# Optimization experiments

Hardware: AMD Instinct MI355X
Metric: run time of the kernel (lower is better)

## Reference

```python
import jax, jax.numpy as jnp
import numpy as np

B, C, QK, T, S = 16, 256, 32, 15, 31


def _conv1x1(x, w, b):
    # 1x1 conv as channel matmul; w: [out, in]
    return jnp.einsum("oc,bchw->bohw", w, x) + b[None, :, None, None]


def _spatial_attn(x, qw, qb, kw, kb, vw, vb, g):
    Bn, Cn, H, W = x.shape
    N = H * W
    q = _conv1x1(x, qw, qb).reshape(Bn, -1, N)  # [B,QK,N]
    k = _conv1x1(x, kw, kb).reshape(Bn, -1, N)  # [B,QK,N]
    v = _conv1x1(x, vw, vb).reshape(Bn, Cn, N)  # [B,C,N]
    energy = jnp.einsum("bqn,bqm->bnm", q, k)   # [B,N,N]
    A = jax.nn.softmax(energy, axis=-1)
    out = g * jnp.einsum("bcm,bnm->bcn", v, A)
    return out.reshape(Bn, Cn, H, W)


def _channel_attn_calc(x):
    Bn, Cn = x.shape[0], x.shape[1]
    f = x.reshape(Bn, Cn, -1)
    e = jnp.einsum("bcn,bdn->bcd", f, f)  # [B,C,C]
    e = jnp.max(e, axis=-1, keepdims=True) - e
    return jax.nn.softmax(e, axis=-1)


def _channel_attn_use(x, A, w):
    Bn, Cn = x.shape[0], x.shape[1]
    v = x.reshape(Bn, Cn, -1)
    return (w * jnp.einsum("bcd,bdn->bcn", A, v)).reshape(x.shape)


def _mod_deform_conv(x, ow, ob, w, b):
    # Modulated deformable conv (DCNv2) 3x3, pad 1, stride 1.
    Bn, Cn, H, W = x.shape
    om = jax.lax.conv_general_dilated(x, ow, (1, 1), ((1, 1), (1, 1)),
                                      dimension_numbers=("NCHW", "OIHW", "NCHW"))
    om = om + ob[None, :, None, None]  # [B,27,H,W]
    off_y, off_x, mask = om[:, :9], om[:, 9:18], jax.nn.sigmoid(om[:, 18:])
    ky, kx = jnp.meshgrid(jnp.arange(3), jnp.arange(3), indexing="ij")
    py = off_y + jnp.arange(H)[None, None, :, None] + (ky.reshape(9) - 1)[None, :, None, None]
    px = off_x + jnp.arange(W)[None, None, None, :] + (kx.reshape(9) - 1)[None, :, None, None]
    y0f = jnp.floor(py); x0f = jnp.floor(px)
    wy = py - y0f; wx = px - x0f
    y0 = y0f.astype(jnp.int32); x0 = x0f.astype(jnp.int32)
    xf = x.reshape(Bn, Cn, H * W)

    def gather(yi, xi, wgt):
        valid = (yi >= 0) & (yi < H) & (xi >= 0) & (xi < W)
        idx = (jnp.clip(yi, 0, H - 1) * W + jnp.clip(xi, 0, W - 1)).reshape(Bn, -1)
        g = jax.vmap(lambda a, i: a[:, i])(xf, idx).reshape(Bn, Cn, 9, H, W)
        return g * (wgt * valid.astype(x.dtype))[:, None]

    val = (gather(y0, x0, (1 - wy) * (1 - wx)) + gather(y0, x0 + 1, (1 - wy) * wx)
           + gather(y0 + 1, x0, wy * (1 - wx)) + gather(y0 + 1, x0 + 1, wy * wx))
    val = val * mask[:, None]  # [B,C,9,H,W]
    return jnp.einsum("bckhw,ock->bohw", val, w.reshape(w.shape[0], Cn, 9)) + b[None, :, None, None]


def _forward(template_features, sr_features,
             t_sp_qw, t_sp_qb, t_sp_kw, t_sp_kb, t_sp_vw, t_sp_vb, t_sp_g,
             s_sp_qw, s_sp_qb, s_sp_kw, s_sp_kb, s_sp_vw, s_sp_vb, s_sp_g,
             w_t_ch, w_s_ch, w_s2t, w_t2s,
             t_off_w, t_off_b, t_dcn_w, t_dcn_b,
             s_off_w, s_off_b, s_dcn_w, s_dcn_b):
    t, s = template_features, sr_features
    t_sp = _spatial_attn(t, t_sp_qw, t_sp_qb, t_sp_kw, t_sp_kb, t_sp_vw, t_sp_vb, t_sp_g)
    s_sp = _spatial_attn(s, s_sp_qw, s_sp_qb, s_sp_kw, s_sp_kb, s_sp_vw, s_sp_vb, s_sp_g)
    tA = _channel_attn_calc(t)
    sA = _channel_attn_calc(s)
    t_ch = _channel_attn_use(t, tA, w_t_ch)
    s_ch = _channel_attn_use(s, sA, w_s_ch)
    t_x = _channel_attn_use(t, sA, w_s2t)   # sr->template cross attention
    s_x = _channel_attn_use(s, tA, w_t2s)   # template->sr cross attention
    t_out = t + t_sp + t_ch + t_x
    s_out = s + s_sp + s_ch + s_x
    t_out = _mod_deform_conv(t_out, t_off_w, t_off_b, t_dcn_w, t_dcn_b)
    s_out = _mod_deform_conv(s_out, s_off_w, s_off_b, s_dcn_w, s_dcn_b)
    return t_out, s_out


def setup_inputs() -> dict:
    key = jax.random.key(0)
    ks = jax.random.split(key, 28)
    r = lambda i, shape, sc=0.05: jax.random.normal(ks[i], shape, dtype=jnp.float32) * sc
    return {
        "template_features": jax.random.normal(ks[0], (B, C, T, T), dtype=jnp.float32),
        "sr_features": jax.random.normal(ks[1], (B, C, S, S), dtype=jnp.float32),
        "t_sp_qw": r(2, (QK, C)), "t_sp_qb": r(3, (QK,)),
        "t_sp_kw": r(4, (QK, C)), "t_sp_kb": r(5, (QK,)),
        "t_sp_vw": r(6, (C, C)), "t_sp_vb": r(7, (C,)), "t_sp_g": r(8, (1,), 0.5),
        "s_sp_qw": r(9, (QK, C)), "s_sp_qb": r(10, (QK,)),
        "s_sp_kw": r(11, (QK, C)), "s_sp_kb": r(12, (QK,)),
        "s_sp_vw": r(13, (C, C)), "s_sp_vb": r(14, (C,)), "s_sp_g": r(15, (1,), 0.5),
        "w_t_ch": r(16, (1,), 0.5), "w_s_ch": r(17, (1,), 0.5),
        "w_s2t": r(18, (1,), 0.5), "w_t2s": r(19, (1,), 0.5),
        "t_off_w": r(20, (27, C, 3, 3), 0.01), "t_off_b": r(21, (27,), 0.01),
        "t_dcn_w": r(22, (C, C, 3, 3)), "t_dcn_b": r(23, (C,)),
        "s_off_w": r(24, (27, C, 3, 3), 0.01), "s_off_b": r(25, (27,), 0.01),
        "s_dcn_w": r(26, (C, C, 3, 3)), "s_dcn_b": r(27, (C,)),
    }


def reference(template_features, sr_features,
              t_sp_qw, t_sp_qb, t_sp_kw, t_sp_kb, t_sp_vw, t_sp_vb, t_sp_g,
              s_sp_qw, s_sp_qb, s_sp_kw, s_sp_kb, s_sp_vw, s_sp_vb, s_sp_g,
              w_t_ch, w_s_ch, w_s2t, w_t2s,
              t_off_w, t_off_b, t_dcn_w, t_dcn_b,
              s_off_w, s_off_b, s_dcn_w, s_dcn_b):
    return _forward(template_features, sr_features,
                    t_sp_qw, t_sp_qb, t_sp_kw, t_sp_kb, t_sp_vw, t_sp_vb, t_sp_g,
                    s_sp_qw, s_sp_qb, s_sp_kw, s_sp_kb, s_sp_vw, s_sp_vb, s_sp_g,
                    w_t_ch, w_s_ch, w_s2t, w_t2s,
                    t_off_w, t_off_b, t_dcn_w, t_dcn_b,
                    s_off_w, s_off_b, s_dcn_w, s_dcn_b)
```

## Files before the change

### kernel.cpp

```cpp
#include <hip/hip_runtime.h>
#include <hip/hip_bf16.h>
#include <cmath>

typedef __attribute__((ext_vector_type(8))) short bf16x8;
typedef __attribute__((ext_vector_type(4))) float f32x4;

__device__ inline ushort f2bf(float f) {
  __hip_bfloat16 h = __float2bfloat16(f);
  return *reinterpret_cast<ushort*>(&h);
}
__device__ inline float bf2f(ushort u) {
  return __uint_as_float((uint)u << 16);
}
__device__ inline float bflo(uint x) { return __uint_as_float(x << 16); }
__device__ inline float bfhi(uint x) { return __uint_as_float(x & 0xffff0000u); }

__device__ inline bool fdecode(int totalS, int gxS, int gyS, int gxT, int gyT,
                               int& bx, int& by, int& bz, bool& isT) {
  const int total = gridDim.x;
  const int id = blockIdx.x;
  int wid = (id & 7) * (total >> 3) + (id >> 3);
  const int totalT = gxT * gyT * 16;
  if (wid >= totalS + totalT) return false;
  isT = wid >= totalS;
  int lid = isT ? wid - totalS : wid;
  const int gx = isT ? gxT : gxS;
  const int gy = isT ? gyT : gyS;
  bx = lid % gx;
  lid /= gx;
  by = lid % gy;
  bz = lid / gy;
  return true;
}

__device__ inline void vdecode(int v, int vtotal, int totalS, int gxS, int gyS,
                               int gxT, int gyT, int& bx, int& by, int& bz,
                               bool& isT) {
  int wid = (v & 7) * (vtotal >> 3) + (v >> 3);
  isT = wid >= totalS;
  int lid = isT ? wid - totalS : wid;
  const int gx = isT ? gxT : gxS;
  const int gy = isT ? gyT : gyS;
  bx = lid % gx;
  lid /= gx;
  by = lid % gy;
  bz = lid / gy;
}

__global__ __launch_bounds__(256) void prep_cast_fused_kernel(
    const float* __restrict__ t_qw, const float* __restrict__ t_qb,
    const float* __restrict__ t_kw, const float* __restrict__ t_kb,
    const float* __restrict__ s_qw, const float* __restrict__ s_qb,
    const float* __restrict__ s_kw, const float* __restrict__ s_kb,
    const float* __restrict__ t_vw, const float* __restrict__ t_vb,
    const float* __restrict__ s_vw, const float* __restrict__ s_vb,
    const float* __restrict__ t_off_w, const float* __restrict__ s_off_w,
    const float* __restrict__ t_dcn_w, const float* __restrict__ s_dcn_w,
    ushort* __restrict__ Wall_t, ushort* __restrict__ Wall_s,
    float* __restrict__ biasAll_t, float* __restrict__ biasAll_s,
    ushort* __restrict__ owb_t, ushort* __restrict__ owb_s,
    ushort* __restrict__ Awb_t, ushort* __restrict__ Awb_s,
    const float* __restrict__ xS, ushort* __restrict__ oS,
    ushort* __restrict__ pS, int NS_, int NRS_, int NpS_,
    const float* __restrict__ xT, ushort* __restrict__ oT,
    ushort* __restrict__ pT, int NT_, int NRT_, int NpT_) {
  __shared__ float T[64][65];
  const int tid = threadIdx.x;
  const int vid = blockIdx.x;
  if (vid < 5832) {
    int i = vid * 256 + tid;
    if (i < 81920) {
      const int r = i >> 8, c = i & 255;
      float v;
      if (r < 256) v = t_vw[(size_t)r * 256 + c];
      else if (r < 288) v = t_qw[(size_t)(r - 256) * 256 + c];
      else v = t_kw[(size_t)(r - 288) * 256 + c];
      Wall_t[i] = f2bf(v);
      return;
    }
    i -= 81920;
    if (i < 81920) {
      const int r = i >> 8, c = i & 255;
      float v;
      if (r < 256) v = s_vw[(size_t)r * 256 + c];
      else if (r < 288) v = s_qw[(size_t)(r - 256) * 256 + c];
      else v = s_kw[(size_t)(r - 288) * 256 + c];
      Wall_s[i] = f2bf(v);
      return;
    }
    i -= 81920;
    if (i < 320) {
      biasAll_t[i] = (i < 256) ? t_vb[i] : ((i < 288) ? t_qb[i - 256] : t_kb[i - 288]);
      return;
    }
    i -= 320;
    if (i < 320) {
      biasAll_s[i] = (i < 256) ? s_vb[i] : ((i < 288) ? s_qb[i - 256] : s_kb[i - 288]);
      return;
    }
    i -= 320;
    if (i < 73728) {
      const int o = i / 2304, k = i % 2304, tap = k >> 8, c = k & 255;
      owb_t[i] = (o < 27) ? f2bf(t_off_w[(size_t)o * 2304 + c * 9 + tap]) : (ushort)0;
      return;
    }
    i -= 73728;
    if (i < 73728) {
      const int o = i / 2304, k = i % 2304, tap = k >> 8, c = k & 255;
      owb_s[i] = (o < 27) ? f2bf(s_off_w[(size_t)o * 2304 + c * 9 + tap]) : (ushort)0;
      return;
    }
    i -= 73728;
    if (i < 589824) {
      const int frag = i >> 9, within = i & 511;
      const int lane = within >> 3, j = within & 7;
      const int mt = frag / 72, kt = frag % 72;
      const int o = mt * 16 + (lane & 15);
      const int k = kt * 32 + (lane >> 4) * 8 + j;
      const int tap = k >> 8, c = k & 255;
      Awb_t[i] = f2bf(t_dcn_w[(size_t)o * 2304 + c * 9 + tap]);
      return;
    }
    i -= 589824;
    if (i < 589824) {
      const int frag = i >> 9, within = i & 511;
      const int lane = within >> 3, j = within & 7;
      const int mt = frag / 72, kt = frag % 72;
      const int o = mt * 16 + (lane & 15);
      const int k = kt * 32 + (lane >> 4) * 8 + j;
      const int tap = k >> 8, c = k & 255;
      Awb_s[i] = f2bf(s_dcn_w[(size_t)o * 2304 + c * 9 + tap]);
    }
    return;
  }
  constexpr int C = 256;
  int bx, by, bz; bool isT;
  vdecode(vid - 5832, 1280, 1024, 16, 4, 4, 4, bx, by, bz, isT);
  const float* x = isT ? xT : xS;
  ushort* xTo = isT ? oT : oS;
  ushort* xbf = isT ? pT : pS;
  const int N = isT ? NT_ : NS_;
  const int NR = isT ? NRT_ : NRS_;
  const int Np = isT ? NpT_ : NpS_;
  const int b = bz;
  const int n0 = bx * 64, c0 = by * 64;
  const float* xb = x + (size_t)b * C * N;
  for (int u = tid; u < 4096; u += 256) {
    const int cc = u >> 6, nn = u & 63;
    const int gn = n0 + nn;
    T[cc][nn] = (gn < N) ? xb[(size_t)(c0 + cc) * N + gn] : 0.f;
  }
  __syncthreads();
  ushort* ob = xTo + (size_t)b * NR * C;
  for (int u = tid; u < 4096; u += 256) {
    const int nn = u >> 6, cc = u & 63;
    ob[(size_t)(n0 + nn) * C + c0 + cc] = f2bf(T[cc][nn]);
  }
  ushort* pb = xbf + (size_t)b * C * Np;
  for (int u = tid; u < 4096; u += 256) {
    const int cc = u >> 6, nn = u & 63;
    const int gn = n0 + nn;
    if (gn < Np) pb[(size_t)(c0 + cc) * Np + gn] = f2bf(T[cc][nn]);
  }
}

__global__ __launch_bounds__(256) void proj_gram_fused_kernel(
    const ushort* __restrict__ WallS, const float* __restrict__ bS,
    const ushort* __restrict__ BtS, ushort* __restrict__ vS,
    float* __restrict__ qkS, int NS_, int NpS_, int NRS_,
    const ushort* __restrict__ WallT, const float* __restrict__ bT,
    const ushort* __restrict__ BtT, ushort* __restrict__ vT,
    float* __restrict__ qkT, int NT_, int NpT_, int NRT_,
    const ushort* __restrict__ xbfS, float* __restrict__ AscP, int KpS_,
    const ushort* __restrict__ xbfT, float* __restrict__ AtcP, int KpT_) {
  constexpr int C = 256;
  __shared__ ushort Asm[128][40];
  __shared__ ushort Bsm[64][40];
  const int tid = threadIdx.x, lane = tid & 63, w = tid >> 6;
  const int vid = blockIdx.x;
  if (vid < 1600) {
    int bx, by, bz; bool isT;
    vdecode(vid, 1600, 1280, 16, 5, 4, 5, bx, by, bz, isT);
    const ushort* Wall = isT ? WallT : WallS;
    const float* bias = isT ? bT : bS;
    const ushort* Bt = isT ? BtT : BtS;
    ushort* vbf = isT ? vT : vS;
    float* qk = isT ? qkT : qkS;
    const int N = isT ? NT_ : NS_, Np = isT ? NpT_ : NpS_, NR = isT ? NRT_ : NRS_;
    const int n0 = bx * 64, m0 = by * 64, b = bz;
    const ushort* Ab = Wall + (size_t)m0 * C;
    const ushort* Bb = Bt + (size_t)b * NR * C;
    f32x4 acc[4];
#pragma unroll
    for (int i = 0; i < 4; i++) acc[i] = (f32x4){0.f, 0.f, 0.f, 0.f};
    for (int k0 = 0; k0 < C; k0 += 32) {
      {
        const int row = tid >> 2, seg = tid & 3;
        *reinterpret_cast<uint4*>(&Asm[row][seg * 8]) =
            *reinterpret_cast<const uint4*>(&Ab[(size_t)row * C + k0 + seg * 8]);
        *reinterpret_cast<uint4*>(&Bsm[row][seg * 8]) =
            *reinterpret_cast<const uint4*>(&Bb[(size_t)(n0 + row) * C + k0 + seg * 8]);
      }
      __syncthreads();
      const int koff = (lane >> 4) * 8;
      const bf16x8 bfr = *reinterpret_cast<const bf16x8*>(&Bsm[w * 16 + (lane & 15)][koff]);
#pragma unroll
      for (int mf = 0; mf < 4; mf++) {
        const bf16x8 af = *reinterpret_cast<const bf16x8*>(&Asm[mf * 16 + (lane & 15)][koff]);
        acc[mf] = __builtin_amdgcn_mfma_f32_16x16x32_bf16(af, bfr, acc[mf], 0, 0, 0);
      }
      __syncthreads();
    }
    const int gn = n0 + w * 16 + (lane & 15);
#pragma unroll
    for (int mf = 0; mf < 4; mf++) {
      const int mbase = m0 + mf * 16 + ((lane >> 4) * 4);
#pragma unroll
      for (int rr = 0; rr < 4; rr++) {
        const int m = mbase + rr;
        if (m < 256) {
          if (gn < Np) {
            ushort v = (gn < N) ? f2bf(acc[mf][rr] + bias[m]) : (ushort)0;
            vbf[((size_t)b * 256 + m) * Np + gn] = v;
          }
        } else {
          if (gn < N)
            qk[((size_t)b * 64 + (m - 256)) * N + gn] = acc[mf][rr] + bias[m];
        }
      }
    }
    return;
  }
  {
    constexpr int BM = 128, NW = 4, NF = 2, WN = 2;
    int bx, by, bz; bool isT;
    vdecode(vid - 1600, 256, 128, 4, 2, 4, 2, bx, by, bz, isT);
    const ushort* A = isT ? xbfT : xbfS;
    float* outF = isT ? AtcP : AscP;
    const int Kp = isT ? KpT_ : KpS_;
    const int n0 = bx * 64, m0 = by * BM, b = bz;
    const ushort* Ab = A + (size_t)b * C * Kp;
    const int wr = w / WN, wc = w % WN;
    f32x4 acc[4][NF];
#pragma unroll
    for (int i = 0; i < 4; i++)
#pragma unroll
      for (int j = 0; j < NF; j++) acc[i][j] = (f32x4){0.f, 0.f, 0.f, 0.f};
    for (int k0 = 0; k0 < Kp; k0 += 32) {
      for (int u = tid; u < BM * 4; u += NW * 64) {
        const int row = u >> 2, seg = u & 3;
        *reinterpret_cast<uint4*>(&Asm[row][seg * 8]) =
            *reinterpret_cast<const uint4*>(&Ab[(size_t)(m0 + row) * Kp + k0 + seg * 8]);
      }
      for (int u = tid; u < 64 * 4; u += NW * 64) {
        const int row = u >> 2, seg = u & 3;
        *reinterpret_cast<uint4*>(&Bsm[row][seg * 8]) =
            *reinterpret_cast<const uint4*>(&Ab[(size_t)(n0 + row) * Kp + k0 + seg * 8]);
      }
      __syncthreads();
      const int koff = (lane >> 4) * 8;
      bf16x8 af[4], bfr[NF];
#pragma unroll
      for (int mf = 0; mf < 4; mf++)
        af[mf] = *reinterpret_cast<const bf16x8*>(&Asm[wr * 64 + mf * 16 + (lane & 15)][koff]);
#pragma unroll
      for (int nf = 0; nf < NF; nf++)
        bfr[nf] = *reinterpret_cast<const bf16x8*>(&Bsm[wc * NF * 16 + nf * 16 + (lane & 15)][koff]);
#pragma unroll
      for (int mf = 0; mf < 4; mf++)
#pragma unroll
        for (int nf = 0; nf < NF; nf++)
          acc[mf][nf] = __builtin_amdgcn_mfma_f32_16x16x32_bf16(af[mf], bfr[nf], acc[mf][nf], 0, 0, 0);
      __syncthreads();
    }
#pragma unroll
    for (int mf = 0; mf < 4; mf++) {
      const int mbase = m0 + wr * 64 + mf * 16 + ((lane >> 4) * 4);
#pragma unroll
      for (int nf = 0; nf < NF; nf++) {
        const int gn = n0 + wc * NF * 16 + nf * 16 + (lane & 15);
#pragma unroll
        for (int rr = 0; rr < 4; rr++)
          outF[((size_t)b * C + mbase + rr) * C + gn] = acc[mf][nf][rr];
      }
    }
  }
}

__global__ __launch_bounds__(256) void energy_mcomb_fused_kernel(
    const float* __restrict__ qkS, ushort* __restrict__ SS, int NS_, int NpS_,
    const float* __restrict__ qkT, ushort* __restrict__ ST, int NT_, int NpT_,
    const float* __restrict__ Atc, const float* __restrict__ Asc,
    const float* __restrict__ w_t_ch, const float* __restrict__ w_s2t,
    const float* __restrict__ w_s_ch, const float* __restrict__ w_t2s,
    ushort* __restrict__ Mc_t, ushort* __restrict__ Mc_s) {
  __shared__ ushort Aq[64][40];
  __shared__ ushort Bk[64][40];
  __shared__ float red[8];
  const int tid = threadIdx.x;
  const int vid = blockIdx.x;
  if (vid < 4352) {
    int bx, by, bz; bool isT;
    vdecode(vid, 4352, 4096, 16, 16, 4, 4, bx, by, bz, isT);
    const float* qk = isT ? qkT : qkS;
    ushort* Sbf = isT ? ST : SS;
    const int N = isT ? NT_ : NS_, Np = isT ? NpT_ : NpS_;
    const int m0 = bx * 64, n0 = by * 64, b = bz;
    const float* qb = qk + (size_t)b * 64 * N;
    const float* kb = qb + (size_t)32 * N;
    const int lane = tid & 63, w = tid >> 6;
    for (int u = tid; u < 2048; u += 256) {
      const int c = u >> 6, nn = u & 63;
      const int gn = n0 + nn, gm = m0 + nn;
      Aq[nn][c] = (gn < N) ? f2bf(qb[(size_t)c * N + gn]) : (ushort)0;
      Bk[nn][c] = (gm < N) ? f2bf(kb[(size_t)c * N + gm]) : (ushort)0;
    }
    __syncthreads();
    const int koff = (lane >> 4) * 8;
    const bf16x8 af = *reinterpret_cast<const bf16x8*>(&Aq[w * 16 + (lane & 15)][koff]);
    f32x4 acc[4];
#pragma unroll
    for (int j = 0; j < 4; j++) {
      const bf16x8 bf = *reinterpret_cast<const bf16x8*>(&Bk[j * 16 + (lane & 15)][koff]);
      acc[j] = __builtin_amdgcn_mfma_f32_16x16x32_bf16(af, bf, (f32x4){0.f, 0.f, 0.f, 0.f}, 0, 0, 0);
    }
#pragma unroll
    for (int j = 0; j < 4; j++) {
      const int m = m0 + j * 16 + (lane & 15);
      if (m >= Np) continue;
#pragma unroll
      for (int r = 0; r < 4; r++) {
        const int n = n0 + w * 16 + (lane >> 4) * 4 + r;
        if (n < N) Sbf[((size_t)b * N + n) * Np + m] = (m < N) ? f2bf(acc[j][r]) : (ushort)0;
      }
    }
    return;
  }
  {
    const int row = vid - 4352;
    const size_t idx = (size_t)row * 256 + tid;
    const float a = -Atc[idx];
    const float s = -Asc[idx];
    float ma = a, ms = s;
#pragma unroll
    for (int off = 32; off; off >>= 1) {
      ma = fmaxf(ma, __shfl_xor(ma, off, 64));
      ms = fmaxf(ms, __shfl_xor(ms, off, 64));
    }
    if ((tid & 63) == 0) { red[tid >> 6] = ma; red[4 + (tid >> 6)] = ms; }
    __syncthreads();
    if (tid == 0) {
      float m1 = red[0], m2 = red[4];
      for (int i = 1; i < 4; i++) { m1 = fmaxf(m1, red[i]); m2 = fmaxf(m2, red[4 + i]); }
      red[0] = m1; red[4] = m2;
    }
    __syncthreads();
    ma = red[0]; ms = red[4];
    __syncthreads();
    const float ea = __expf(a - ma), es = __expf(s - ms);
    float sa = ea, ss = es;
#pragma unroll
    for (int off = 32; off; off >>= 1) {
      sa += __shfl_xor(sa, off, 64);
      ss += __shfl_xor(ss, off, 64);
    }
    if ((tid & 63) == 0) { red[tid >> 6] = sa; red[4 + (tid >> 6)] = ss; }
    __syncthreads();
    if (tid == 0) {
      float t1 = 0.f, t2 = 0.f;
      for (int i = 0; i < 4; i++) { t1 += red[i]; t2 += red[4 + i]; }
      red[0] = t1; red[4] = t2;
    }
    __syncthreads();
    const float Pa = ea / red[0], Ps = es / red[4];
    Mc_t[idx] = f2bf(w_t_ch[0] * Pa + w_s2t[0] * Ps);
    Mc_s[idx] = f2bf(w_s_ch[0] * Ps + w_t2s[0] * Pa);
  }
}

__global__ __launch_bounds__(256) void softmax_bf16_fused_kernel(
    ushort* __restrict__ Ss, int Ns, int Nps, ushort* __restrict__ St, int Nt,
    int Npt, int rowsS) {
  __shared__ float buf[992];
  __shared__ float red[4];
  const int row = blockIdx.x;
  ushort* r;
  int N;
  if (row < rowsS) {
    r = Ss + (size_t)row * Nps;
    N = Ns;
  } else {
    r = St + (size_t)(row - rowsS) * Npt;
    N = Nt;
  }
  const int tid = threadIdx.x;
  float mx = -1e30f;
  for (int i = tid; i < N; i += 256) {
    float f = bf2f(r[i]);
    buf[i] = f;
    mx = fmaxf(mx, f);
  }
#pragma unroll
  for (int off = 32; off; off >>= 1) mx = fmaxf(mx, __shfl_xor(mx, off, 64));
  if ((tid & 63) == 0) red[tid >> 6] = mx;
  __syncthreads();
  if (tid == 0) {
    float m2 = red[0];
    for (int i = 1; i < 4; i++) m2 = fmaxf(m2, red[i]);
    red[0] = m2;
  }
  __syncthreads();
  mx = red[0];
  __syncthreads();
  float s = 0.f;
  for (int i = tid; i < N; i += 256) {
    float v = __expf(buf[i] - mx);
    buf[i] = v;
    s += v;
  }
#pragma unroll
  for (int off = 32; off; off >>= 1) s += __shfl_xor(s, off, 64);
  if ((tid & 63) == 0) red[tid >> 6] = s;
  __syncthreads();
  if (tid == 0) {
    float t = 0.f;
    for (int i = 0; i < 4; i++) t += red[i];
    red[0] = t;
  }
  __syncthreads();
  const float inv = 1.f / red[0];
  for (int i = tid; i < N; i += 256) r[i] = f2bf(buf[i] * inv);
}

__global__ __launch_bounds__(256) void pv_chan_fused_kernel(
    const ushort* __restrict__ vS, const ushort* __restrict__ SS,
    const ushort* __restrict__ McS, const ushort* __restrict__ xTS,
    const float* __restrict__ xS, const float* __restrict__ gS,
    ushort* __restrict__ xsTS, int NS_, int NpS_, int NRS_,
    const ushort* __restrict__ vT, const ushort* __restrict__ ST,
    const ushort* __restrict__ McT, const ushort* __restrict__ xTT,
    const float* __restrict__ xT_, const float* __restrict__ gT,
    ushort* __restrict__ xsTT, int NT_, int NpT_, int NRT_) {
  constexpr int C = 256, BM = 128, NW = 4, NF = 2, WN = 2;
  __shared__ ushort Asm[BM][40];
  __shared__ ushort Bsm[64][40];
  int bx, by, bz; bool isT;
  if (!fdecode(512, 16, 2, 4, 2, bx, by, bz, isT)) return;
  const ushort* vbf = isT ? vT : vS;
  const ushort* Sbf = isT ? ST : SS;
  const ushort* Mc = isT ? McT : McS;
  const ushort* xTb = isT ? xTT : xTS;
  const float* x = isT ? xT_ : xS;
  const float* gp = isT ? gT : gS;
  ushort* xsT = isT ? xsTT : xsTS;
  const int N = isT ? NT_ : NS_, Np = isT ? NpT_ : NpS_;
  const int NR = isT ? NRT_ : NRS_;
  const int n0 = bx * 64, m0 = by * BM, b = bz;
  const int tid = threadIdx.x, lane = tid & 63, w = tid >> 6;
  const int wr = w / WN, wc = w % WN;
  f32x4 acc[4][NF];
#pragma unroll
  for (int i = 0; i < 4; i++)
#pragma unroll
    for (int j = 0; j < NF; j++) acc[i][j] = (f32x4){0.f, 0.f, 0.f, 0.f};
  const int koff = (lane >> 4) * 8;
  {
    const ushort* Ab = vbf + (size_t)b * C * Np;
    const ushort* Bb = Sbf + (size_t)b * (size_t)N * Np;
    for (int k0 = 0; k0 < Np; k0 += 32) {
      for (int u = tid; u < BM * 4; u += NW * 64) {
        const int row = u >> 2, seg = u & 3;
        *reinterpret_cast<uint4*>(&Asm[row][seg * 8]) =
            *reinterpret_cast<const uint4*>(&Ab[(size_t)(m0 + row) * Np + k0 + seg * 8]);
      }
      for (int u = tid; u < 64 * 4; u += NW * 64) {
        const int row = u >> 2, seg = u & 3;
        const int gn = n0 + row;
        uint4 val;
        if (gn < N)
          val = *reinterpret_cast<const uint4*>(&Bb[(size_t)gn * Np + k0 + seg * 8]);
        else
          val = make_uint4(0, 0, 0, 0);
        *reinterpret_cast<uint4*>(&Bsm[row][seg * 8]) = val;
      }
      __syncthreads();
      bf16x8 af[4], bfr[NF];
#pragma unroll
      for (int mf = 0; mf < 4; mf++)
        af[mf] = *reinterpret_cast<const bf16x8*>(&Asm[wr * 64 + mf * 16 + (lane & 15)][koff]);
#pragma unroll
      for (int nf = 0; nf < NF; nf++)
        bfr[nf] = *reinterpret_cast<const bf16x8*>(&Bsm[wc * NF * 16 + nf * 16 + (lane & 15)][koff]);
#pragma unroll
      for (int mf = 0; mf < 4; mf++)
#pragma unroll
        for (int nf = 0; nf < NF; nf++)
          acc[mf][nf] = __builtin_amdgcn_mfma_f32_16x16x32_bf16(af[mf], bfr[nf], acc[mf][nf], 0, 0, 0);
      __syncthreads();
    }
  }
  const float g = *gp;
#pragma unroll
  for (int mf = 0; mf < 4; mf++)
#pragma unroll
    for (int nf = 0; nf < NF; nf++)
#pragma unroll
      for (int rr = 0; rr < 4; rr++) acc[mf][nf][rr] *= g;
  {
    const ushort* Ab = Mc + (size_t)b * C * C;
    const ushort* Bb = xTb + (size_t)b * NR * C;
    for (int k0 = 0; k0 < C; k0 += 32) {
      for (int u = tid; u < BM * 4; u += NW * 64) {
        const int row = u >> 2, seg = u & 3;
        *reinterpret_cast<uint4*>(&Asm[row][seg * 8]) =
            *reinterpret_cast<const uint4*>(&Ab[(size_t)(m0 + row) * C + k0 + seg * 8]);
      }
      for (int u = tid; u < 64 * 4; u += NW * 64) {
        const int row = u >> 2, seg = u & 3;
        *reinterpret_cast<uint4*>(&Bsm[row][seg * 8]) =
            *reinterpret_cast<const uint4*>(&Bb[(size_t)(n0 + row) * C + k0 + seg * 8]);
      }
      __syncthreads();
      bf16x8 af[4], bfr[NF];
#pragma unroll
      for (int mf = 0; mf < 4; mf++)
        af[mf] = *reinterpret_cast<const bf16x8*>(&Asm[wr * 64 + mf * 16 + (lane & 15)][koff]);
#pragma unroll
      for (int nf = 0; nf < NF; nf++)
        bfr[nf] = *reinterpret_cast<const bf16x8*>(&Bsm[wc * NF * 16 + nf * 16 + (lane & 15)][koff]);
#pragma unroll
      for (int mf = 0; mf < 4; mf++)
#pragma unroll
        for (int nf = 0; nf < NF; nf++)
          acc[mf][nf] = __builtin_amdgcn_mfma_f32_16x16x32_bf16(af[mf], bfr[nf], acc[mf][nf], 0, 0, 0);
      __syncthreads();
    }
  }
#pragma unroll
  for (int mf = 0; mf < 4; mf++) {
    const int mbase = m0 + wr * 64 + mf * 16 + ((lane >> 4) * 4);
#pragma unroll
    for (int nf = 0; nf < NF; nf++) {
      const int gn = n0 + wc * NF * 16 + nf * 16 + (lane & 15);
      if (gn < N) {
        float s[4];
#pragma unroll
        for (int rr = 0; rr < 4; rr++)
          s[rr] = x[((size_t)b * C + mbase + rr) * N + gn] + acc[mf][nf][rr];
        uint lo = (uint)f2bf(s[0]) | ((uint)f2bf(s[1]) << 16);
        uint hi = (uint)f2bf(s[2]) | ((uint)f2bf(s[3]) << 16);
        *reinterpret_cast<uint2*>(&xsT[((size_t)b * NR + gn) * C + mbase]) =
            make_uint2(lo, hi);
      }
    }
  }
}

__global__ __launch_bounds__(256) void offconv_prep_fused_kernel(
    const ushort* __restrict__ xS, const ushort* __restrict__ owS,
    const float* __restrict__ obS, uint4* __restrict__ prS, int HS_, int WS_,
    int NS_, int NRS_,
    const ushort* __restrict__ xT, const ushort* __restrict__ owT,
    const float* __restrict__ obT, uint4* __restrict__ prT, int HT_, int WT_,
    int NT_, int NRT_) {
  __shared__ ushort Asm[32][136];
  __shared__ ushort Bsm[64][136];
  __shared__ int qsrc[64];
  __shared__ float som[27][65];
  int bx, by, bz; bool isT;
  if (!fdecode(256, 16, 1, 4, 1, bx, by, bz, isT)) return;
  const ushort* xsT = isT ? xT : xS;
  const ushort* owb = isT ? owT : owS;
  const float* ob = isT ? obT : obS;
  uint4* prep = isT ? prT : prS;
  const int H = isT ? HT_ : HS_, Wd = isT ? WT_ : WS_;
  const int N = isT ? NT_ : NS_, NR = isT ? NRT_ : NRS_;
  const int n0 = bx * 64, b = bz;
  const int tid = threadIdx.x, lane = tid & 63, w = tid >> 6;
  const ushort* xb = xsT + (size_t)b * NR * 256;
  f32x4 acc[2];
  acc[0] = (f32x4){0.f, 0.f, 0.f, 0.f};
  acc[1] = (f32x4){0.f, 0.f, 0.f, 0.f};
  for (int tap = 0; tap < 9; ++tap) {
    const int dy = tap / 3 - 1, dx = tap - (tap / 3) * 3 - 1;
    if (tid < 64) {
      const int p = n0 + tid;
      int q = -1;
      if (p < N) {
        const int h = p / Wd, ww = p - (p / Wd) * Wd;
        const int yy = h + dy, xx = ww + dx;
        if (yy >= 0 && yy < H && xx >= 0 && xx < Wd) q = yy * Wd + xx;
      }
      qsrc[tid] = q;
    }
    __syncthreads();
#pragma unroll
    for (int half = 0; half < 2; ++half) {
      const int k0 = tap * 256 + half * 128;
      for (int u = tid; u < 512; u += 256) {
        const int row = u >> 4, seg = u & 15;
        *reinterpret_cast<uint4*>(&Asm[row][seg * 8]) =
            *reinterpret_cast<const uint4*>(&owb[(size_t)row * 2304 + k0 + seg * 8]);
      }
      for (int u = tid; u < 1024; u += 256) {
        const int row = u >> 4, seg = u & 15;
        const int q = qsrc[row];
        uint4 val = make_uint4(0, 0, 0, 0);
        if (q >= 0)
          val = *reinterpret_cast<const uint4*>(&xb[(size_t)q * 256 + half * 128 + seg * 8]);
        *reinterpret_cast<uint4*>(&Bsm[row][seg * 8]) = val;
      }
      __syncthreads();
#pragma unroll
      for (int sub = 0; sub < 4; ++sub) {
        const int koff = sub * 32 + (lane >> 4) * 8;
        const bf16x8 b0 = *reinterpret_cast<const bf16x8*>(&Bsm[w * 16 + (lane & 15)][koff]);
#pragma unroll
        for (int mf = 0; mf < 2; ++mf) {
          const bf16x8 a0 = *reinterpret_cast<const bf16x8*>(&Asm[mf * 16 + (lane & 15)][koff]);
          acc[mf] = __builtin_amdgcn_mfma_f32_16x16x32_bf16(a0, b0, acc[mf], 0, 0, 0);
        }
      }
      __syncthreads();
    }
  }
#pragma unroll
  for (int mf = 0; mf < 2; ++mf) {
#pragma unroll
    for (int r = 0; r < 4; ++r) {
      const int o = mf * 16 + (lane >> 4) * 4 + r;
      const int n = w * 16 + (lane & 15);
      if (o < 27) som[o][n] = acc[mf][r] + ob[o];
    }
  }
  __syncthreads();
  for (int u = tid; u < 576; u += 256) {
    const int tap = u / 64, pp = u - (u / 64) * 64;
    const int p = n0 + pp;
    if (p >= N) continue;
    const float offy = som[tap][pp];
    const float offx = som[9 + tap][pp];
    const float mraw = som[18 + tap][pp];
    const float mval = 1.f / (1.f + __expf(-mraw));
    const int ky = tap / 3, kx = tap - (tap / 3) * 3;
    const int h = p / Wd, ww = p - (p / Wd) * Wd;
    const float py = offy + (float)(h + ky - 1);
    const float px = offx + (float)(ww + kx - 1);
    const float y0f = floorf(py), x0f = floorf(px);
    const float wy = py - y0f, wx = px - x0f;
    const int y0 = (int)y0f, x0 = (int)x0f;
    const int ys0 = min(max(y0, 0), H - 2);
    const int xs0 = min(max(x0, 0), Wd - 2);
    const float wr0 = (ys0 == y0) ? (1.f - wy) : ((ys0 == y0 + 1) ? wy : 0.f);
    const float wr1 = (ys0 + 1 == y0) ? (1.f - wy) : ((ys0 + 1 == y0 + 1) ? wy : 0.f);
    const float wc0 = (xs0 == x0) ? (1.f - wx) : ((xs0 == x0 + 1) ? wx : 0.f);
    const float wc1 = (xs0 + 1 == x0) ? (1.f - wx) : ((xs0 + 1 == x0 + 1) ? wx : 0.f);
    const float w00 = wr0 * wc0 * mval, w01 = wr0 * wc1 * mval;
    const float w10 = wr1 * wc0 * mval, w11 = wr1 * wc1 * mval;
    uint4 pk;
    pk.x = (uint)(ys0 * Wd + xs0);
    pk.y = (uint)f2bf(w00) | ((uint)f2bf(w01) << 16);
    pk.z = (uint)f2bf(w10) | ((uint)f2bf(w11) << 16);
    pk.w = 0;
    prep[((size_t)b * 9 + tap) * N + p] = pk;
  }
}

__global__ __launch_bounds__(512) void dcn_fused_kernel(
    const ushort* __restrict__ xS, const uint4* __restrict__ prS,
    const ushort* __restrict__ AwS, const float* __restrict__ biS,
    float* __restrict__ oS, int NS_, int WS_, int NRS_,
    const ushort* __restrict__ xT, const uint4* __restrict__ prT,
    const ushort* __restrict__ AwT, const float* __restrict__ biT,
    float* __restrict__ oT, int NT_, int WT_, int NRT_) {
  constexpr int C = 256, MF = 4;
  __shared__ ushort Bsm[32][72];
  __shared__ int sq[32];
  __shared__ float swl[4][32];
  int bx, by, bz; bool isT;
  if (!fdecode(512, 32, 1, 8, 1, bx, by, bz, isT)) return;
  const ushort* xsT = isT ? xT : xS;
  const uint4* prep = isT ? prT : prS;
  const ushort* Awb = isT ? AwT : AwS;
  const float* bias = isT ? biT : biS;
  float* out = isT ? oT : oS;
  const int N = isT ? NT_ : NS_, Wd = isT ? WT_ : WS_, NR = isT ? NRT_ : NRS_;
  const int n0 = bx * 32, b = bz;
  const int tid = threadIdx.x, lane = tid & 63, w = tid >> 6;
  const int wr = w >> 1, wc = w & 1;
  const ushort* xb = xsT + (size_t)b * NR * C;
  const int un0 = tid >> 5;
  const int un1 = un0 + 16;
  const int kk2 = (tid & 31) * 2;
  f32x4 acc[MF];
#pragma unroll
  for (int i = 0; i < MF; i++) acc[i] = (f32x4){0.f, 0.f, 0.f, 0.f};
  uint bReg[2][4];
  int sqr0 = 0, sqr1 = 0;
  float w0a[4], w1a[4];
  const size_t rowYp = (size_t)Wd * C;
  for (int tap = 0; tap < 9; ++tap) {
    if (tid < 32) {
      const int p = n0 + tid;
      if (p < N) {
        const uint4 pk = prep[((size_t)b * 9 + tap) * N + p];
        sq[tid] = (int)pk.x * C;
        swl[0][tid] = bf2f((ushort)(pk.y & 0xffff));
        swl[1][tid] = bf2f((ushort)(pk.y >> 16));
        swl[2][tid] = bf2f((ushort)(pk.z & 0xffff));
        swl[3][tid] = bf2f((ushort)(pk.z >> 16));
      } else {
        sq[tid] = 0;
        swl[0][tid] = swl[1][tid] = swl[2][tid] = swl[3][tid] = 0.f;
      }
    }
    __syncthreads();
    sqr0 = sq[un0];
    sqr1 = sq[un1];
#pragma unroll
    for (int q = 0; q < 4; q++) {
      w0a[q] = swl[q][un0];
      w1a[q] = swl[q][un1];
    }
    {
      const ushort* pA = xb + sqr0 + kk2;
      bReg[0][0] = *reinterpret_cast<const uint*>(pA);
      bReg[0][1] = *reinterpret_cast<const uint*>(pA + C);
      bReg[0][2] = *reinterpret_cast<const uint*>(pA + rowYp);
      bReg[0][3] = *reinterpret_cast<const uint*>(pA + rowYp + C);
      const ushort* pB = xb + sqr1 + kk2;
      bReg[1][0] = *reinterpret_cast<const uint*>(pB);
      bReg[1][1] = *reinterpret_cast<const uint*>(pB + C);
      bReg[1][2] = *reinterpret_cast<const uint*>(pB + rowYp);
      bReg[1][3] = *reinterpret_cast<const uint*>(pB + rowYp + C);
    }
#pragma unroll
    for (int ks = 0; ks < 4; ++ks) {
      bf16x8 afr[2][4];
      const int ktb = tap * 8 + ks * 2;
#pragma unroll
      for (int sub = 0; sub < 2; ++sub)
#pragma unroll
        for (int mf = 0; mf < 4; ++mf)
          afr[sub][mf] = *reinterpret_cast<const bf16x8*>(
              Awb + ((((size_t)(wr * 4 + mf) * 72) + ktb + sub) << 9) + lane * 8);
      {
        const float vlo0 = w0a[0] * bflo(bReg[0][0]) + w0a[1] * bflo(bReg[0][1]) +
                           w0a[2] * bflo(bReg[0][2]) + w0a[3] * bflo(bReg[0][3]);
        const float vhi0 = w0a[0] * bfhi(bReg[0][0]) + w0a[1] * bfhi(bReg[0][1]) +
                           w0a[2] * bfhi(bReg[0][2]) + w0a[3] * bfhi(bReg[0][3]);
        *reinterpret_cast<uint*>(&Bsm[un0][kk2]) =
            (uint)f2bf(vlo0) | ((uint)f2bf(vhi0) << 16);
        const float vlo1 = w1a[0] * bflo(bReg[1][0]) + w1a[1] * bflo(bReg[1][1]) +
                           w1a[2] * bflo(bReg[1][2]) + w1a[3] * bflo(bReg[1][3]);
        const float vhi1 = w1a[0] * bfhi(bReg[1][0]) + w1a[1] * bfhi(bReg[1][1]) +
                           w1a[2] * bfhi(bReg[1][2]) + w1a[3] * bfhi(bReg[1][3]);
        *reinterpret_cast<uint*>(&Bsm[un1][kk2]) =
            (uint)f2bf(vlo1) | ((uint)f2bf(vhi1) << 16);
      }
      __syncthreads();
      if (ks < 3) {
        const int c1 = (ks + 1) * 64;
        const ushort* pA = xb + sqr0 + c1 + kk2;
        bReg[0][0] = *reinterpret_cast<const uint*>(pA);
        bReg[0][1] = *reinterpret_cast<const uint*>(pA + C);
        bReg[0][2] = *reinterpret_cast<const uint*>(pA + rowYp);
        bReg[0][3] = *reinterpret_cast<const uint*>(pA + rowYp + C);
        const ushort* pB = xb + sqr1 + c1 + kk2;
        bReg[1][0] = *reinterpret_cast<const uint*>(pB);
        bReg[1][1] = *reinterpret_cast<const uint*>(pB + C);
        bReg[1][2] = *reinterpret_cast<const uint*>(pB + rowYp);
        bReg[1][3] = *reinterpret_cast<const uint*>(pB + rowYp + C);
      }
#pragma unroll
      for (int sub = 0; sub < 2; ++sub) {
        const int koff = sub * 32 + (lane >> 4) * 8;
        const bf16x8 bfv = *reinterpret_cast<const bf16x8*>(&Bsm[wc * 16 + (lane & 15)][koff]);
#pragma unroll
        for (int mf = 0; mf < MF; mf++)
          acc[mf] = __builtin_amdgcn_mfma_f32_16x16x32_bf16(afr[sub][mf], bfv, acc[mf], 0, 0, 0);
      }
      __syncthreads();
    }
  }
  const int gn = n0 + wc * 16 + (lane & 15);
#pragma unroll
  for (int mf = 0; mf < MF; mf++) {
    const int mbase = wr * 64 + mf * 16 + ((lane >> 4) * 4);
    if (gn < N) {
#pragma unroll
      for (int rr = 0; rr < 4; rr++)
        out[((size_t)b * C + mbase + rr) * N + gn] = acc[mf][rr] + bias[mbase + rr];
    }
  }
}

extern "C" void kernel_launch(void* const* d_in, const int* in_sizes, int n_in,
                              void* d_out, int out_size, void* d_ws, size_t ws_size,
                              hipStream_t stream) {
  const float* t_in = (const float*)d_in[0];
  const float* s_in = (const float*)d_in[1];
  const float* t_qw = (const float*)d_in[2];
  const float* t_qb = (const float*)d_in[3];
  const float* t_kw = (const float*)d_in[4];
  const float* t_kb = (const float*)d_in[5];
  const float* t_vw = (const float*)d_in[6];
  const float* t_vb = (const float*)d_in[7];
  const float* t_g = (const float*)d_in[8];
  const float* s_qw = (const float*)d_in[9];
  const float* s_qb = (const float*)d_in[10];
  const float* s_kw = (const float*)d_in[11];
  const float* s_kb = (const float*)d_in[12];
  const float* s_vw = (const float*)d_in[13];
  const float* s_vb = (const float*)d_in[14];
  const float* s_g = (const float*)d_in[15];
  const float* w_t_ch = (const float*)d_in[16];
  const float* w_s_ch = (const float*)d_in[17];
  const float* w_s2t = (const float*)d_in[18];
  const float* w_t2s = (const float*)d_in[19];
  const float* t_off_w = (const float*)d_in[20];
  const float* t_off_b = (const float*)d_in[21];
  const float* t_dcn_w = (const float*)d_in[22];
  const float* t_dcn_b = (const float*)d_in[23];
  const float* s_off_w = (const float*)d_in[24];
  const float* s_off_b = (const float*)d_in[25];
  const float* s_dcn_w = (const float*)d_in[26];
  const float* s_dcn_b = (const float*)d_in[27];
  (void)in_sizes; (void)n_in; (void)out_size; (void)ws_size;

  constexpr int Bn = 16, C = 256;
  constexpr int HT = 15, WT = 15, NT = HT * WT;
  constexpr int HS = 31, WS2 = 31, NS = HS * WS2;
  constexpr int NpT = 256, NpS = 992;
  constexpr int NRT = 256, NRS = 1024;

  float* ws = (float*)d_ws;
  size_t off = 0;
  auto alloc = [&](size_t n) {
    n = (n + 3) & ~(size_t)3;
    float* p = ws + off; off += n; return p;
  };
  auto allocU = [&](size_t nu) { return (ushort*)alloc((nu + 1) / 2); };

  float* qk_t = alloc((size_t)Bn * 64 * NT);
  float* qk_s = alloc((size_t)Bn * 64 * NS);
  ushort* Wall_t = allocU((size_t)320 * C);
  ushort* Wall_s = allocU((size_t)320 * C);
  float* biasAll_t = alloc(320);
  float* biasAll_s = alloc(320);
  ushort* xT_t = allocU((size_t)Bn * NRT * C);
  ushort* xT_s = allocU((size_t)Bn * NRS * C);
  ushort* xbf_t = allocU((size_t)Bn * C * NpT);
  ushort* xbf_s = allocU((size_t)Bn * C * NpS);
  ushort* v_tbf = allocU((size_t)Bn * C * NpT);
  ushort* v_sbf = allocU((size_t)Bn * C * NpS);
  ushort* S_t = allocU((size_t)Bn * NT * NpT);
  ushort* S_s = allocU((size_t)Bn * NS * NpS);
  ushort* xsT_t = allocU((size_t)Bn * NRT * C);
  ushort* xsT_s = allocU((size_t)Bn * NRS * C);
  float* Atc = alloc((size_t)Bn * C * C);
  float* Asc = alloc((size_t)Bn * C * C);
  ushort* Mc_t = allocU((size_t)Bn * C * C);
  ushort* Mc_s = allocU((size_t)Bn * C * C);
  ushort* owb_t = allocU((size_t)32 * 2304);
  ushort* owb_s = allocU((size_t)32 * 2304);
  ushort* Awb_t = allocU((size_t)256 * 2304);
  ushort* Awb_s = allocU((size_t)256 * 2304);
  uint4* prep_t = (uint4*)alloc((size_t)Bn * 9 * NT * 4);
  uint4* prep_s = (uint4*)alloc((size_t)Bn * 9 * NS * 4);

  dim3 blk(256);

  prep_cast_fused_kernel<<<dim3(5832 + 1280), blk, 0, stream>>>(
      t_qw, t_qb, t_kw, t_kb, s_qw, s_qb, s_kw, s_kb,
      t_vw, t_vb, s_vw, s_vb, t_off_w, s_off_w, t_dcn_w, s_dcn_w,
      Wall_t, Wall_s, biasAll_t, biasAll_s, owb_t, owb_s, Awb_t, Awb_s,
      s_in, xT_s, xbf_s, NS, NRS, NpS, t_in, xT_t, xbf_t, NT, NRT, NpT);

  proj_gram_fused_kernel<<<dim3(1600 + 256), blk, 0, stream>>>(
      Wall_s, biasAll_s, xT_s, v_sbf, qk_s, NS, NpS, NRS,
      Wall_t, biasAll_t, xT_t, v_tbf, qk_t, NT, NpT, NRT,
      xbf_s, Asc, NpS, xbf_t, Atc, NpT);

  energy_mcomb_fused_kernel<<<dim3(4352 + 4096), blk, 0, stream>>>(
      qk_s, S_s, NS, NpS, qk_t, S_t, NT, NpT,
      Atc, Asc, w_t_ch, w_s2t, w_s_ch, w_t2s, Mc_t, Mc_s);

  softmax_bf16_fused_kernel<<<dim3(Bn * NS + Bn * NT), blk, 0, stream>>>(
      S_s, NS, NpS, S_t, NT, NpT, Bn * NS);

  pv_chan_fused_kernel<<<dim3(640), blk, 0, stream>>>(
      v_sbf, S_s, Mc_s, xT_s, s_in, s_g, xsT_s, NS, NpS, NRS,
      v_tbf, S_t, Mc_t, xT_t, t_in, t_g, xsT_t, NT, NpT, NRT);

  offconv_prep_fused_kernel<<<dim3(320), blk, 0, stream>>>(
      xsT_s, owb_s, s_off_b, prep_s, HS, WS2, NS, NRS,
      xsT_t, owb_t, t_off_b, prep_t, HT, WT, NT, NRT);

  float* out_t = (float*)d_out;
  float* out_s = out_t + (size_t)Bn * C * NT;
  dcn_fused_kernel<<<dim3(640), dim3(512), 0, stream>>>(
      xsT_s, prep_s, Awb_s, s_dcn_b, out_s, NS, WS2, NRS,
      xsT_t, prep_t, Awb_t, t_dcn_b, out_t, NT, WT, NRT);
}
```

Before: 273.3 us.

## Fuse spatial softmax into energy and PV kernels via deferred normalization

```diff
diff --git a/kernel.cpp b/kernel.cpp
--- a/kernel.cpp
+++ b/kernel.cpp
@@ -63,7 +63,8 @@
     const float* __restrict__ xS, ushort* __restrict__ oS,
     ushort* __restrict__ pS, int NS_, int NRS_, int NpS_,
     const float* __restrict__ xT, ushort* __restrict__ oT,
-    ushort* __restrict__ pT, int NT_, int NRT_, int NpT_) {
+    ushort* __restrict__ pT, int NT_, int NRT_, int NpT_,
+    float* __restrict__ rsS, float* __restrict__ rsT) {
   __shared__ float T[64][65];
   const int tid = threadIdx.x;
   const int vid = blockIdx.x;
@@ -131,6 +132,12 @@
       const int tap = k >> 8, c = k & 255;
       Awb_s[i] = f2bf(s_dcn_w[(size_t)o * 2304 + c * 9 + tap]);
     }
+    return;
+  }
+  if (vid >= 7112) {
+    int i = (vid - 7112) * 256 + tid;
+    if (i < 15376) rsS[i] = 0.f;
+    else if (i < 18976) rsT[i - 15376] = 0.f;
     return;
   }
   constexpr int C = 256;
@@ -290,6 +297,7 @@
 __global__ __launch_bounds__(256) void energy_mcomb_fused_kernel(
     const float* __restrict__ qkS, ushort* __restrict__ SS, int NS_, int NpS_,
     const float* __restrict__ qkT, ushort* __restrict__ ST, int NT_, int NpT_,
+    float* __restrict__ rsS, float* __restrict__ rsT,
     const float* __restrict__ Atc, const float* __restrict__ Asc,
     const float* __restrict__ w_t_ch, const float* __restrict__ w_s2t,
     const float* __restrict__ w_s_ch, const float* __restrict__ w_t2s,
@@ -304,6 +312,7 @@
     vdecode(vid, 4352, 4096, 16, 16, 4, 4, bx, by, bz, isT);
     const float* qk = isT ? qkT : qkS;
     ushort* Sbf = isT ? ST : SS;
+    float* rowsum = isT ? rsT : rsS;
     const int N = isT ? NT_ : NS_, Np = isT ? NpT_ : NpS_;
     const int m0 = bx * 64, n0 = by * 64, b = bz;
     const float* qb = qk + (size_t)b * 64 * N;
@@ -324,14 +333,29 @@
       const bf16x8 bf = *reinterpret_cast<const bf16x8*>(&Bk[j * 16 + (lane & 15)][koff]);
       acc[j] = __builtin_amdgcn_mfma_f32_16x16x32_bf16(af, bf, (f32x4){0.f, 0.f, 0.f, 0.f}, 0, 0, 0);
     }
+    float psum[4] = {0.f, 0.f, 0.f, 0.f};
 #pragma unroll
     for (int j = 0; j < 4; j++) {
       const int m = m0 + j * 16 + (lane & 15);
-      if (m >= Np) continue;
 #pragma unroll
       for (int r = 0; r < 4; r++) {
         const int n = n0 + w * 16 + (lane >> 4) * 4 + r;
-        if (n < N) Sbf[((size_t)b * N + n) * Np + m] = (m < N) ? f2bf(acc[j][r]) : (ushort)0;
+        float e = 0.f;
+        if (m < N) e = __expf(acc[j][r]);
+        if (m < Np && n < N) Sbf[((size_t)b * N + n) * Np + m] = f2bf(e);
+        psum[r] += e;
+      }
+    }
+#pragma unroll
+    for (int d = 1; d < 16; d <<= 1) {
+#pragma unroll
+      for (int r = 0; r < 4; r++) psum[r] += __shfl_xor(psum[r], d, 64);
+    }
+    if ((lane & 15) == 0) {
+#pragma unroll
+      for (int r = 0; r < 4; r++) {
+        const int n = n0 + w * 16 + (lane >> 4) * 4 + r;
+        if (n < N) atomicAdd(&rowsum[(size_t)b * N + n], psum[r]);
       }
     }
     return;
@@ -378,69 +402,17 @@
   }
 }
 
-__global__ __launch_bounds__(256) void softmax_bf16_fused_kernel(
-    ushort* __restrict__ Ss, int Ns, int Nps, ushort* __restrict__ St, int Nt,
-    int Npt, int rowsS) {
-  __shared__ float buf[992];
-  __shared__ float red[4];
-  const int row = blockIdx.x;
-  ushort* r;
-  int N;
-  if (row < rowsS) {
-    r = Ss + (size_t)row * Nps;
-    N = Ns;
-  } else {
-    r = St + (size_t)(row - rowsS) * Npt;
-    N = Nt;
-  }
-  const int tid = threadIdx.x;
-  float mx = -1e30f;
-  for (int i = tid; i < N; i += 256) {
-    float f = bf2f(r[i]);
-    buf[i] = f;
-    mx = fmaxf(mx, f);
-  }
-#pragma unroll
-  for (int off = 32; off; off >>= 1) mx = fmaxf(mx, __shfl_xor(mx, off, 64));
-  if ((tid & 63) == 0) red[tid >> 6] = mx;
-  __syncthreads();
-  if (tid == 0) {
-    float m2 = red[0];
-    for (int i = 1; i < 4; i++) m2 = fmaxf(m2, red[i]);
-    red[0] = m2;
-  }
-  __syncthreads();
-  mx = red[0];
-  __syncthreads();
-  float s = 0.f;
-  for (int i = tid; i < N; i += 256) {
-    float v = __expf(buf[i] - mx);
-    buf[i] = v;
-    s += v;
-  }
-#pragma unroll
-  for (int off = 32; off; off >>= 1) s += __shfl_xor(s, off, 64);
-  if ((tid & 63) == 0) red[tid >> 6] = s;
-  __syncthreads();
-  if (tid == 0) {
-    float t = 0.f;
-    for (int i = 0; i < 4; i++) t += red[i];
-    red[0] = t;
-  }
-  __syncthreads();
-  const float inv = 1.f / red[0];
-  for (int i = tid; i < N; i += 256) r[i] = f2bf(buf[i] * inv);
-}
-
 __global__ __launch_bounds__(256) void pv_chan_fused_kernel(
     const ushort* __restrict__ vS, const ushort* __restrict__ SS,
-    const ushort* __restrict__ McS, const ushort* __restrict__ xTS,
-    const float* __restrict__ xS, const float* __restrict__ gS,
-    ushort* __restrict__ xsTS, int NS_, int NpS_, int NRS_,
+    const float* __restrict__ rsS, const ushort* __restrict__ McS,
+    const ushort* __restrict__ xTS, const float* __restrict__ xS,
+    const float* __restrict__ gS, ushort* __restrict__ xsTS, int NS_,
+    int NpS_, int NRS_,
     const ushort* __restrict__ vT, const ushort* __restrict__ ST,
-    const ushort* __restrict__ McT, const ushort* __restrict__ xTT,
-    const float* __restrict__ xT_, const float* __restrict__ gT,
-    ushort* __restrict__ xsTT, int NT_, int NpT_, int NRT_) {
+    const float* __restrict__ rsT, const ushort* __restrict__ McT,
+    const ushort* __restrict__ xTT, const float* __restrict__ xT_,
+    const float* __restrict__ gT, ushort* __restrict__ xsTT, int NT_,
+    int NpT_, int NRT_) {
   constexpr int C = 256, BM = 128, NW = 4, NF = 2, WN = 2;
   __shared__ ushort Asm[BM][40];
   __shared__ ushort Bsm[64][40];
@@ -448,6 +420,7 @@
   if (!fdecode(512, 16, 2, 4, 2, bx, by, bz, isT)) return;
   const ushort* vbf = isT ? vT : vS;
   const ushort* Sbf = isT ? ST : SS;
+  const float* rowsum = isT ? rsT : rsS;
   const ushort* Mc = isT ? McT : McS;
   const ushort* xTb = isT ? xTT : xTS;
   const float* x = isT ? xT_ : xS;
@@ -500,12 +473,19 @@
     }
   }
   const float g = *gp;
+  float fac[NF];
+#pragma unroll
+  for (int nf = 0; nf < NF; nf++) {
+    const int gn = n0 + wc * NF * 16 + nf * 16 + (lane & 15);
+    const float rs = (gn < N) ? rowsum[(size_t)b * N + gn] : 1.f;
+    fac[nf] = g / rs;
+  }
 #pragma unroll
   for (int mf = 0; mf < 4; mf++)
 #pragma unroll
     for (int nf = 0; nf < NF; nf++)
 #pragma unroll
-      for (int rr = 0; rr < 4; rr++) acc[mf][nf][rr] *= g;
+      for (int rr = 0; rr < 4; rr++) acc[mf][nf][rr] *= fac[nf];
   {
     const ushort* Ab = Mc + (size_t)b * C * C;
     const ushort* Bb = xTb + (size_t)b * NR * C;
@@ -856,6 +836,8 @@
   ushort* v_sbf = allocU((size_t)Bn * C * NpS);
   ushort* S_t = allocU((size_t)Bn * NT * NpT);
   ushort* S_s = allocU((size_t)Bn * NS * NpS);
+  float* rs_t = alloc((size_t)Bn * NT);
+  float* rs_s = alloc((size_t)Bn * NS);
   ushort* xsT_t = allocU((size_t)Bn * NRT * C);
   ushort* xsT_s = allocU((size_t)Bn * NRS * C);
   float* Atc = alloc((size_t)Bn * C * C);
@@ -871,11 +853,12 @@
 
   dim3 blk(256);
 
-  prep_cast_fused_kernel<<<dim3(5832 + 1280), blk, 0, stream>>>(
+  prep_cast_fused_kernel<<<dim3(5832 + 1280 + 75), blk, 0, stream>>>(
       t_qw, t_qb, t_kw, t_kb, s_qw, s_qb, s_kw, s_kb,
       t_vw, t_vb, s_vw, s_vb, t_off_w, s_off_w, t_dcn_w, s_dcn_w,
       Wall_t, Wall_s, biasAll_t, biasAll_s, owb_t, owb_s, Awb_t, Awb_s,
-      s_in, xT_s, xbf_s, NS, NRS, NpS, t_in, xT_t, xbf_t, NT, NRT, NpT);
+      s_in, xT_s, xbf_s, NS, NRS, NpS, t_in, xT_t, xbf_t, NT, NRT, NpT,
+      rs_s, rs_t);
 
   proj_gram_fused_kernel<<<dim3(1600 + 256), blk, 0, stream>>>(
       Wall_s, biasAll_s, xT_s, v_sbf, qk_s, NS, NpS, NRS,
@@ -883,15 +866,12 @@
       xbf_s, Asc, NpS, xbf_t, Atc, NpT);
 
   energy_mcomb_fused_kernel<<<dim3(4352 + 4096), blk, 0, stream>>>(
-      qk_s, S_s, NS, NpS, qk_t, S_t, NT, NpT,
+      qk_s, S_s, NS, NpS, qk_t, S_t, NT, NpT, rs_s, rs_t,
       Atc, Asc, w_t_ch, w_s2t, w_s_ch, w_t2s, Mc_t, Mc_s);
 
-  softmax_bf16_fused_kernel<<<dim3(Bn * NS + Bn * NT), blk, 0, stream>>>(
-      S_s, NS, NpS, S_t, NT, NpT, Bn * NS);
-
   pv_chan_fused_kernel<<<dim3(640), blk, 0, stream>>>(
-      v_sbf, S_s, Mc_s, xT_s, s_in, s_g, xsT_s, NS, NpS, NRS,
-      v_tbf, S_t, Mc_t, xT_t, t_in, t_g, xsT_t, NT, NpT, NRT);
+      v_sbf, S_s, rs_s, Mc_s, xT_s, s_in, s_g, xsT_s, NS, NpS, NRS,
+      v_tbf, S_t, rs_t, Mc_t, xT_t, t_in, t_g, xsT_t, NT, NpT, NRT);
 
   offconv_prep_fused_kernel<<<dim3(320), blk, 0, stream>>>(
       xsT_s, owb_s, s_off_b, prep_s, HS, WS2, NS, NRS,
```

Measured after the change: 256.7 us. -6.1%, faster.
